# Kernel optimization log

Measured on AMD Instinct MI355X. Metric: run time of the kernel, lower is better.

The kernel has to match this reference:

```python
import jax, jax.numpy as jnp
import numpy as np

K = 3000          # number of clusters (init default)
K_SPARSE = 128    # top-k sparsification width (sparse_dim / cluster_config.k_sparse)
LR = 0.2          # EMA learning rate used in train()
EPS = 1e-12       # F.normalize eps


def setup_inputs() -> dict:
    key = jax.random.key(0)
    kx, km = jax.random.split(key)
    x = jax.random.normal(kx, (65536, 768), dtype=jnp.float32)
    mu = jax.random.normal(km, (K, 768), dtype=jnp.float32)
    mu = mu / jnp.maximum(jnp.linalg.norm(mu, axis=-1, keepdims=True), EPS)
    return {"x": x, "mu": mu}


def reference(x, mu):
    k, d = mu.shape
    # train() appends the current centers to each batch so no cluster is empty
    data = jnp.concatenate([x, mu], axis=0)            # (n+k, d)
    n_tot = data.shape[0]

    # get_r: inner-product argmax assignment
    sim = data @ mu.T                                  # (n+k, k)
    r = jnp.argmax(sim, axis=1)
    r = r.at[-k:].set(jnp.arange(k))                   # force one member per cluster

    # get_mu, vectorized: segment mean that drops the LAST member when count > 1
    ones = jnp.ones((n_tot,), dtype=data.dtype)
    counts = jax.ops.segment_sum(ones, r, num_segments=k)          # (k,)
    sums = jax.ops.segment_sum(data, r, num_segments=k)            # (k, d)
    last_idx = jax.ops.segment_max(jnp.arange(n_tot), r, num_segments=k)
    x_last = data[last_idx]                                        # (k, d)
    cnt = counts[:, None]
    u = jnp.where(cnt > 1,
                  (sums - x_last) / jnp.maximum(cnt - 1.0, 1.0),
                  sums / jnp.maximum(cnt, 1.0))

    # EMA update + normalize
    u = u * LR + mu * (1.0 - LR)
    u = u / jnp.maximum(jnp.linalg.norm(u, axis=-1, keepdims=True), EPS)

    # top_k_sparse(u, K_SPARSE).to_dense(): keep top-K_SPARSE entries by magnitude per row
    th = jax.lax.top_k(jnp.abs(u), K_SPARSE)[0][:, -1:]            # (k, 1)
    u = jnp.where(jnp.abs(u) >= th, u, jnp.zeros((), u.dtype))

    dis = jnp.max(jnp.linalg.norm(u - mu, axis=-1))
    return u, dis
```

## Files before the change

### kernel.cpp

```cpp
#include <hip/hip_runtime.h>
#include <hip/hip_bf16.h>

#define M 65536
#define N 3000
#define NPAD 3072
#define K 768
#define NT_K 24
#define NTIL 24
#define KSP 128
#define MAXL 8192
#define GAPTHR 8e-3f
#define MAXAMB 16384
#define MAXWL 196608
#define NEGINF -3.4e38f

typedef __attribute__((ext_vector_type(8))) _Float16 f16x8;
typedef __attribute__((ext_vector_type(4))) float f32x4;
typedef unsigned long long u64;
typedef unsigned int u32;

#define AS1 __attribute__((address_space(1)))
#define AS3 __attribute__((address_space(3)))

#define OFF_A2   0ull
#define OFF_B2   100663296ull
#define OFF_GTOP 105381888ull
#define OFF_RB   130547712ull
#define OFF_R    131072000ull
#define OFF_AMB  131334144ull
#define OFF_WL   131465216ull
#define OFF_CNT  132251648ull
#define WS_NEED  132251904ull

__device__ inline unsigned short f2h(float x) {
  _Float16 h = (_Float16)x;
  return *reinterpret_cast<unsigned short*>(&h);
}
__device__ inline u32 fkey(float v) {
  u32 ub = __float_as_uint(v);
  return (ub & 0x80000000u) ? ~ub : (ub | 0x80000000u);
}
__device__ inline float keyf(u32 key) {
  u32 ub = (key & 0x80000000u) ? (key ^ 0x80000000u) : ~key;
  return __uint_as_float(ub);
}
__device__ inline void gload16(const void* g, void* l) {
  __builtin_amdgcn_global_load_lds((AS1 u32*)g, (AS3 u32*)l, 16, 0, 0);
}

__global__ __launch_bounds__(256) void k_convx(const float* __restrict__ X,
                                               unsigned short* __restrict__ A2) {
  const int tot = M * (K / 8);
  for (int i = blockIdx.x * 256 + threadIdx.x; i < tot; i += gridDim.x * 256) {
    size_t base = (size_t)i * 8;
    float4 v0 = *reinterpret_cast<const float4*>(X + base);
    float4 v1 = *reinterpret_cast<const float4*>(X + base + 4);
    ushort4 h0, h1;
    h0.x = f2h(v0.x); h0.y = f2h(v0.y); h0.z = f2h(v0.z); h0.w = f2h(v0.w);
    h1.x = f2h(v1.x); h1.y = f2h(v1.y); h1.z = f2h(v1.z); h1.w = f2h(v1.w);
    *reinterpret_cast<ushort4*>(A2 + base) = h0;
    *reinterpret_cast<ushort4*>(A2 + base + 4) = h1;
  }
}

__global__ __launch_bounds__(256) void k_convmu(const float* __restrict__ MU,
                                                unsigned short* __restrict__ B2,
                                                u32* __restrict__ cnts,
                                                float* __restrict__ dis_slot) {
  int j = blockIdx.x, t = threadIdx.x;
  if (j == 0 && t == 0) { cnts[0] = 0u; cnts[1] = 0u; }
  if (j == 0 && t == 1) *dis_slot = 0.0f;
  for (int c = t; c < K; c += 256) {
    float x = (j < N) ? MU[(size_t)j * K + c] : 0.0f;
    B2[(size_t)j * K + c] = f2h(x);
  }
}

__global__ __launch_bounds__(256, 4) void k_gemm(const unsigned short* __restrict__ A2,
                                                 const unsigned short* __restrict__ B2,
                                                 u64* __restrict__ gtop) {
  __shared__ unsigned short smem[16384];

  const int bid = blockIdx.x;
  const int xcd = bid & 7, idx = bid >> 3;
  const int g = idx / 96, rem = idx % 96;
  const int nt = rem >> 2, mi = rem & 3;
  const int mt = xcd * 64 + g * 4 + mi;
  const int m0 = mt * 128, n0 = nt * 128;

  const int t = threadIdx.x;
  const int w = t >> 6, ln = t & 63;
  const int wr = w >> 1, wc = w & 1;
  const int li = ln & 15, lg = ln >> 4;

  const int r0 = t >> 2;
  const int c0 = ((t & 3) ^ ((t >> 3) & 3)) * 8;
  const unsigned short* pa0 = A2 + (size_t)(m0 + r0) * K + c0;
  const unsigned short* pb0 = B2 + (size_t)(n0 + r0) * K + c0;

  f32x4 acc[4][4] = {};

  const int rA = wr * 64 + li;
  const int rB = wc * 64 + li;
  const int cc = (lg ^ ((li >> 1) & 3)) * 8;

#define STAGE(kt_, p_)                                                        \
  {                                                                           \
    int k0_ = (kt_) * 32;                                                     \
    gload16(pa0 + k0_, smem + (p_) * 4096 + t * 8);                           \
    gload16(pa0 + (size_t)64 * K + k0_, smem + (p_) * 4096 + 2048 + t * 8);   \
    gload16(pb0 + k0_, smem + 8192 + (p_) * 4096 + t * 8);                    \
    gload16(pb0 + (size_t)64 * K + k0_,                                       \
            smem + 8192 + (p_) * 4096 + 2048 + t * 8);                        \
  }

  STAGE(0, 0);
  STAGE(1, 1);

  for (int kt = 0; kt < NT_K; ++kt) {
    const int p = kt & 1;
    if (kt >= NT_K - 1)
      asm volatile("s_waitcnt vmcnt(0)" ::: "memory");
    else
      asm volatile("s_waitcnt vmcnt(4)" ::: "memory");
    __builtin_amdgcn_s_barrier();
    asm volatile("" ::: "memory");

    const unsigned short* baseA = smem + p * 4096;
    const unsigned short* baseB = smem + 8192 + p * 4096;
    f16x8 aa[4], bb[4];
#pragma unroll
    for (int n_ = 0; n_ < 4; ++n_)
      bb[n_] = *reinterpret_cast<const f16x8*>(baseB + (rB + n_ * 16) * 32 + cc);
#pragma unroll
    for (int m_ = 0; m_ < 4; ++m_)
      aa[m_] = *reinterpret_cast<const f16x8*>(baseA + (rA + m_ * 16) * 32 + cc);

    __builtin_amdgcn_s_setprio(1);
#pragma unroll
    for (int m_ = 0; m_ < 4; ++m_)
#pragma unroll
      for (int n_ = 0; n_ < 4; ++n_)
        acc[m_][n_] = __builtin_amdgcn_mfma_f32_16x16x32_f16(
            aa[m_], bb[n_], acc[m_][n_], 0, 0, 0);
    __builtin_amdgcn_s_setprio(0);

    asm volatile("s_waitcnt lgkmcnt(0)" ::: "memory");
    __builtin_amdgcn_s_barrier();
    asm volatile("" ::: "memory");
    if (kt < NT_K - 2) STAGE(kt + 2, p);
  }

  u64* stop = reinterpret_cast<u64*>(smem);
#pragma unroll
  for (int m = 0; m < 4; ++m)
#pragma unroll
    for (int reg = 0; reg < 4; ++reg) {
      float l1 = NEGINF, l2 = NEGINF;
      int nb = 0;
#pragma unroll
      for (int n = 0; n < 4; ++n) {
        int col = n0 + wc * 64 + n * 16 + li;
        float v = (col < N) ? acc[m][n][reg] : NEGINF;
        if (v > l1) { l2 = l1; l1 = v; nb = n; }
        else if (v > l2) l2 = v;
      }
      const float loc1 = l1;
#pragma unroll
      for (int s = 1; s < 16; s <<= 1) {
        float o1 = __shfl_xor(l1, s, 64);
        float o2 = __shfl_xor(l2, s, 64);
        float hi = fmaxf(l1, o1);
        float lo = fminf(l1, o1);
        l2 = fmaxf(lo, fmaxf(l2, o2));
        l1 = hi;
      }
      unsigned long long bal = __ballot(loc1 == l1);
      unsigned mask16 = (unsigned)(bal >> (lg * 16)) & 0xffffu;
      int first = __builtin_ctz(mask16 | 0x10000u);
      int nbo = __shfl(nb, lg * 16 + first, 64);
      int col1 = n0 + wc * 64 + nbo * 16 + first;
      if (li == 0) {
        int rloc = wr * 64 + m * 16 + lg * 4 + reg;
        stop[(wc * 128 + rloc) * 2 + 0] =
            ((u64)fkey(l1) << 32) | (u32)(~(u32)col1);
        stop[(wc * 128 + rloc) * 2 + 1] = ((u64)fkey(l2) << 32);
      }
    }
  __syncthreads();
  if (t < 128) {
    u64 g1 = 0, g2 = 0;
#pragma unroll
    for (int q = 0; q < 2; ++q) {
      u64 a1 = stop[(q * 128 + t) * 2 + 0], a2 = stop[(q * 128 + t) * 2 + 1];
      u64 n1 = g1 > a1 ? g1 : a1;
      u64 lo = g1 > a1 ? a1 : g1;
      u64 mx = g2 > a2 ? g2 : a2;
      g2 = lo > mx ? lo : mx;
      g1 = n1;
    }
    u64* dst = gtop + ((size_t)(m0 + t) * NTIL + nt) * 2;
    dst[0] = g1;
    dst[1] = g2;
  }
}

__global__ __launch_bounds__(256) void k_reduce(const u64* __restrict__ gtop,
                                                int* __restrict__ r,
                                                int* __restrict__ amb,
                                                u64* __restrict__ rbest,
                                                u32* __restrict__ wl,
                                                u32* __restrict__ cnts) {
  int row = blockIdx.x * 256 + threadIdx.x;
  if (row >= M) return;
  const u64* src = gtop + (size_t)row * NTIL * 2;
  u64 tops[NTIL];
  u64 g1 = 0, g2 = 0;
#pragma unroll
  for (int tt = 0; tt < NTIL; ++tt) {
    u64 a1 = src[tt * 2], a2 = src[tt * 2 + 1];
    tops[tt] = a1;
    u64 n1 = g1 > a1 ? g1 : a1;
    u64 lo = g1 > a1 ? a1 : g1;
    u64 mx = g2 > a2 ? g2 : a2;
    g2 = lo > mx ? lo : mx;
    g1 = n1;
  }
  r[row] = (int)(~(u32)(g1 & 0xffffffffull));
  float v1 = keyf((u32)(g1 >> 32)), v2 = keyf((u32)(g2 >> 32));
  if (v1 - v2 < GAPTHR) {
    u32 idx = atomicAdd(&cnts[0], 1u);
    if (idx < MAXAMB) {
      amb[idx] = row;
      rbest[row] = 0ull;
      float thr = v1 - GAPTHR;
#pragma unroll
      for (int tt = 0; tt < NTIL; ++tt) {
        if (keyf((u32)(tops[tt] >> 32)) >= thr) {
          u32 wi = atomicAdd(&cnts[1], 1u);
          if (wi < MAXWL) wl[wi] = ((u32)row << 5) | (u32)tt;
        }
      }
    }
  }
}

__global__ __launch_bounds__(256) void k_refine(const float* __restrict__ X,
                                                const float* __restrict__ MU,
                                                const u32* __restrict__ wl,
                                                const u32* __restrict__ cnts,
                                                u64* __restrict__ rbest) {
  __shared__ float xrow[768];
  __shared__ u64 wb[4];
  const int t = threadIdx.x, w = t >> 6, ln = t & 63;
  const int nw = (int)min(cnts[1], (u32)MAXWL);
  for (int u = blockIdx.x; u < nw; u += gridDim.x) {
    const u32 e = wl[u];
    const int row = (int)(e >> 5), tile = (int)(e & 31);

    xrow[t] = X[(size_t)row * K + t];
    xrow[t + 256] = X[(size_t)row * K + t + 256];
    xrow[t + 512] = X[(size_t)row * K + t + 512];
    __syncthreads();

    u64 best = 0;
    for (int q = 0; q < 8; ++q) {
      const int cbase = tile * 128 + w * 32 + q * 4;
      const float* m0p = MU + (size_t)min(cbase + 0, N - 1) * K;
      const float* m1p = MU + (size_t)min(cbase + 1, N - 1) * K;
      const float* m2p = MU + (size_t)min(cbase + 2, N - 1) * K;
      const float* m3p = MU + (size_t)min(cbase + 3, N - 1) * K;
      float p0 = 0.f, p1 = 0.f, p2 = 0.f, p3 = 0.f;
#pragma unroll
      for (int it = 0; it < 3; ++it) {
        int d4 = (ln + it * 64) * 4;
        float4 xv = *reinterpret_cast<const float4*>(&xrow[d4]);
        float4 a0 = *reinterpret_cast<const float4*>(m0p + d4);
        float4 a1 = *reinterpret_cast<const float4*>(m1p + d4);
        float4 a2 = *reinterpret_cast<const float4*>(m2p + d4);
        float4 a3 = *reinterpret_cast<const float4*>(m3p + d4);
        p0 += xv.x * a0.x + xv.y * a0.y + xv.z * a0.z + xv.w * a0.w;
        p1 += xv.x * a1.x + xv.y * a1.y + xv.z * a1.z + xv.w * a1.w;
        p2 += xv.x * a2.x + xv.y * a2.y + xv.z * a2.z + xv.w * a2.w;
        p3 += xv.x * a3.x + xv.y * a3.y + xv.z * a3.z + xv.w * a3.w;
      }
#pragma unroll
      for (int s = 32; s; s >>= 1) {
        p0 += __shfl_xor(p0, s, 64);
        p1 += __shfl_xor(p1, s, 64);
        p2 += __shfl_xor(p2, s, 64);
        p3 += __shfl_xor(p3, s, 64);
      }
      if (ln == 0) {
        float ps[4] = {p0, p1, p2, p3};
#pragma unroll
        for (int i = 0; i < 4; ++i) {
          int c = cbase + i;
          if (c < N) {
            u64 pk = ((u64)fkey(ps[i]) << 32) | (u32)(~(u32)c);
            if (pk > best) best = pk;
          }
        }
      }
    }
    if (ln == 0) wb[w] = best;
    __syncthreads();
    if (t == 0) {
      u64 b = wb[0];
#pragma unroll
      for (int i = 1; i < 4; ++i)
        if (wb[i] > b) b = wb[i];
      atomicMax(&rbest[row], b);
    }
    __syncthreads();
  }
}

__global__ __launch_bounds__(256) void k_decode2(const int* __restrict__ amb,
                                                 const u64* __restrict__ rbest,
                                                 const u32* __restrict__ cnts,
                                                 int* __restrict__ r) {
  int i = blockIdx.x * 256 + threadIdx.x;
  int n_amb = (int)min(cnts[0], (u32)MAXAMB);
  if (i < n_amb) {
    int row = amb[i];
    r[row] = (int)(~(u32)(rbest[row] & 0xffffffffull));
  }
}

__global__ __launch_bounds__(256) void k_finalize(const float* __restrict__ X,
                                                  const float* __restrict__ MU,
                                                  const int* __restrict__ r,
                                                  float* __restrict__ out,
                                                  float* __restrict__ dis_slot) {
#pragma clang fp contract(off)
  const int j = blockIdx.x;
  const int t = threadIdx.x;
  const int lane = t & 63;
  const int wid = t >> 6;
  __shared__ int list[MAXL];
  __shared__ int wc4[4][4];
  __shared__ float red[4];
  __shared__ unsigned hist[256];
  __shared__ int selI;

  int cnt = 0;
  for (int base = 0; base < M; base += 1024) {
    bool f[4];
    u64 bm[4];
#pragma unroll
    for (int q = 0; q < 4; ++q) {
      f[q] = (r[base + q * 256 + t] == j);
      bm[q] = __ballot(f[q]);
    }
    if (lane == 0) {
#pragma unroll
      for (int q = 0; q < 4; ++q) wc4[wid][q] = __popcll(bm[q]);
    }
    __syncthreads();
    int goff = cnt;
#pragma unroll
    for (int q = 0; q < 4; ++q) {
      if (f[q]) {
        int off = goff;
        for (int ww = 0; ww < wid; ++ww) off += wc4[ww][q];
        int pos = off + __popcll(bm[q] & ((1ull << lane) - 1ull));
        if (pos < MAXL) list[pos] = base + q * 256 + t;
      }
      goff += wc4[0][q] + wc4[1][q] + wc4[2][q] + wc4[3][q];
    }
    cnt = goff;
    __syncthreads();
  }
  int cl = cnt < MAXL ? cnt : MAXL;

  float a0 = 0.f, a1 = 0.f, a2 = 0.f, a3 = 0.f;
  float b0 = 0.f, b1 = 0.f, b2 = 0.f, b3 = 0.f;
  float c0 = 0.f, c1 = 0.f, c2 = 0.f, c3 = 0.f;
  int m = 0;
  for (; m + 3 < cl; m += 4) {
    const float* x0 = X + (size_t)list[m + 0] * K;
    const float* x1 = X + (size_t)list[m + 1] * K;
    const float* x2 = X + (size_t)list[m + 2] * K;
    const float* x3 = X + (size_t)list[m + 3] * K;
    a0 += x0[t]; b0 += x0[t + 256]; c0 += x0[t + 512];
    a1 += x1[t]; b1 += x1[t + 256]; c1 += x1[t + 512];
    a2 += x2[t]; b2 += x2[t + 256]; c2 += x2[t + 512];
    a3 += x3[t]; b3 += x3[t + 256]; c3 += x3[t + 512];
  }
  for (; m < cl; ++m) {
    const float* xr = X + (size_t)list[m] * K;
    a0 += xr[t]; b0 += xr[t + 256]; c0 += xr[t + 512];
  }
  float s0 = ((a0 + a1) + a2) + a3;
  float s1 = ((b0 + b1) + b2) + b3;
  float s2 = ((c0 + c1) + c2) + c3;

  const float mu0 = MU[(size_t)j * K + t];
  const float mu1 = MU[(size_t)j * K + t + 256];
  const float mu2 = MU[(size_t)j * K + t + 512];

  float u0, u1, u2;
  if (cnt >= 1) {
    float c = (float)cnt;
    u0 = s0 / c; u1 = s1 / c; u2 = s2 / c;
  } else {
    u0 = mu0; u1 = mu1; u2 = mu2;
  }
  float v0 = u0 * 0.2f + mu0 * 0.8f;
  float v1 = u1 * 0.2f + mu1 * 0.8f;
  float v2 = u2 * 0.2f + mu2 * 0.8f;

  float ss = v0 * v0 + v1 * v1 + v2 * v2;
#pragma unroll
  for (int s = 32; s > 0; s >>= 1) ss += __shfl_down(ss, s, 64);
  if (lane == 0) red[wid] = ss;
  __syncthreads();
  float tot = red[0] + red[1] + red[2] + red[3];
  float den = sqrtf(tot);
  den = fmaxf(den, 1e-12f);
  float un0 = v0 / den, un1 = v1 / den, un2 = v2 / den;
  unsigned k0b = __float_as_uint(fabsf(un0));
  unsigned k1b = __float_as_uint(fabsf(un1));
  unsigned k2b = __float_as_uint(fabsf(un2));
  __syncthreads();

  unsigned cur = 0;
  int need = KSP;
  for (int sh = 24; sh >= 0; sh -= 8) {
    hist[t] = 0u;
    if (t == 0) selI = -1;
    __syncthreads();
    bool m0_ = (sh == 24) || ((k0b >> (sh + 8)) == (cur >> (sh + 8)));
    bool m1_ = (sh == 24) || ((k1b >> (sh + 8)) == (cur >> (sh + 8)));
    bool m2_ = (sh == 24) || ((k2b >> (sh + 8)) == (cur >> (sh + 8)));
    if (m0_) atomicAdd(&hist[(k0b >> sh) & 255u], 1u);
    if (m1_) atomicAdd(&hist[(k1b >> sh) & 255u], 1u);
    if (m2_) atomicAdd(&hist[(k2b >> sh) & 255u], 1u);
    __syncthreads();
#pragma unroll
    for (int off = 1; off < 256; off <<= 1) {
      unsigned nb = (t + off < 256) ? hist[t + off] : 0u;
      __syncthreads();
      hist[t] += nb;
      __syncthreads();
    }
    if (hist[t] >= (unsigned)need) atomicMax(&selI, t);
    __syncthreads();
    int b = selI < 0 ? 0 : selI;
    unsigned above = (b < 255) ? hist[b + 1] : 0u;
    cur |= ((unsigned)b << sh);
    need = need - (int)above;
    __syncthreads();
  }
  unsigned th = cur;

  float o0 = (k0b >= th) ? un0 : 0.0f;
  float o1 = (k1b >= th) ? un1 : 0.0f;
  float o2 = (k2b >= th) ? un2 : 0.0f;
  out[(size_t)j * K + t] = o0;
  out[(size_t)j * K + t + 256] = o1;
  out[(size_t)j * K + t + 512] = o2;

  float q0 = o0 - mu0, q1 = o1 - mu1, q2 = o2 - mu2;
  float dq = q0 * q0 + q1 * q1 + q2 * q2;
#pragma unroll
  for (int s = 32; s > 0; s >>= 1) dq += __shfl_down(dq, s, 64);
  __syncthreads();
  if (lane == 0) red[wid] = dq;
  __syncthreads();
  if (t == 0) {
    float dtot = red[0] + red[1] + red[2] + red[3];
    float dn = sqrtf(dtot);
    atomicMax((unsigned*)dis_slot, __float_as_uint(dn));
  }
}

__global__ __launch_bounds__(256) void k0_init(u64* __restrict__ best,
                                               float* __restrict__ dis_slot) {
  int i = blockIdx.x * 256 + threadIdx.x;
  if (i < M) best[i] = 0ull;
  if (i == 0) *dis_slot = 0.0f;
}

__global__ __launch_bounds__(256) void k1_f32(const float* __restrict__ X,
                                              const float* __restrict__ MU,
                                              u64* __restrict__ best) {
  __shared__ float Asf[16][64];
  __shared__ float Bsf[16][64];
  const int m0 = blockIdx.x * 64;
  const int n0 = blockIdx.y * 64;
  const int t = threadIdx.x;
  const int tx = t & 15, ty = t >> 4;
  const int lrow = t >> 2, lcg = t & 3;

  float acc[4][4];
#pragma unroll
  for (int i = 0; i < 4; ++i)
#pragma unroll
    for (int jj = 0; jj < 4; ++jj) acc[i][jj] = 0.0f;

  const float* aptr = X + (size_t)(m0 + lrow) * K + lcg * 4;
  const bool bvalid = (n0 + lrow) < N;
  const float* bptr = MU + (size_t)(bvalid ? (n0 + lrow) : 0) * K + lcg * 4;

  for (int k0 = 0; k0 < K; k0 += 16) {
    float4 av = *reinterpret_cast<const float4*>(aptr + k0);
    float4 bv = make_float4(0.f, 0.f, 0.f, 0.f);
    if (bvalid) bv = *reinterpret_cast<const float4*>(bptr + k0);
    Asf[lcg * 4 + 0][lrow] = av.x; Asf[lcg * 4 + 1][lrow] = av.y;
    Asf[lcg * 4 + 2][lrow] = av.z; Asf[lcg * 4 + 3][lrow] = av.w;
    Bsf[lcg * 4 + 0][lrow] = bv.x; Bsf[lcg * 4 + 1][lrow] = bv.y;
    Bsf[lcg * 4 + 2][lrow] = bv.z; Bsf[lcg * 4 + 3][lrow] = bv.w;
    __syncthreads();
#pragma unroll
    for (int kk = 0; kk < 16; ++kk) {
      float4 af = *reinterpret_cast<const float4*>(&Asf[kk][ty * 4]);
      float4 bf = *reinterpret_cast<const float4*>(&Bsf[kk][tx * 4]);
      float a[4] = {af.x, af.y, af.z, af.w};
      float b[4] = {bf.x, bf.y, bf.z, bf.w};
#pragma unroll
      for (int i = 0; i < 4; ++i)
#pragma unroll
        for (int jj = 0; jj < 4; ++jj)
          acc[i][jj] = fmaf(a[i], b[jj], acc[i][jj]);
    }
    __syncthreads();
  }
#pragma unroll
  for (int i = 0; i < 4; ++i) {
    u64 bk = 0ull;
#pragma unroll
    for (int jj = 0; jj < 4; ++jj) {
      int col = n0 + tx * 4 + jj;
      if (col < N) {
        u64 pk = ((u64)fkey(acc[i][jj]) << 32) | (u32)(~(u32)col);
        if (pk > bk) bk = pk;
      }
    }
#pragma unroll
    for (int s = 1; s < 16; s <<= 1) {
      u64 o = __shfl_xor((unsigned long long)bk, s, 64);
      if (o > bk) bk = o;
    }
    if (tx == 0) atomicMax(&best[m0 + ty * 4 + i], bk);
  }
}

__global__ __launch_bounds__(256) void k2_decode(const u64* __restrict__ best,
                                                 int* __restrict__ r) {
  int i = blockIdx.x * 256 + threadIdx.x;
  if (i < M) r[i] = (int)(~(u32)(best[i] & 0xffffffffull));
}

extern "C" void kernel_launch(void* const* d_in, const int* in_sizes, int n_in,
                              void* d_out, int out_size, void* d_ws, size_t ws_size,
                              hipStream_t stream) {
  const float* X = (const float*)d_in[0];
  const float* MU = (const float*)d_in[1];
  float* out = (float*)d_out;
  float* dis_slot = out + (size_t)N * K;

  if (ws_size >= WS_NEED) {
    unsigned short* A2 = (unsigned short*)((char*)d_ws + OFF_A2);
    unsigned short* B2 = (unsigned short*)((char*)d_ws + OFF_B2);
    u64* gtop = (u64*)((char*)d_ws + OFF_GTOP);
    u64* rbest = (u64*)((char*)d_ws + OFF_RB);
    int* r = (int*)((char*)d_ws + OFF_R);
    int* amb = (int*)((char*)d_ws + OFF_AMB);
    u32* wl = (u32*)((char*)d_ws + OFF_WL);
    u32* cnts = (u32*)((char*)d_ws + OFF_CNT);

    k_convx<<<8192, 256, 0, stream>>>(X, A2);
    k_convmu<<<NPAD, 256, 0, stream>>>(MU, B2, cnts, dis_slot);
    k_gemm<<<512 * NTIL, 256, 0, stream>>>(A2, B2, gtop);
    k_reduce<<<M / 256, 256, 0, stream>>>(gtop, r, amb, rbest, wl, cnts);
    k_refine<<<2048, 256, 0, stream>>>(X, MU, wl, cnts, rbest);
    k_decode2<<<MAXAMB / 256, 256, 0, stream>>>(amb, rbest, cnts, r);
    k_finalize<<<N, 256, 0, stream>>>(X, MU, r, out, dis_slot);
  } else {
    u64* best = (u64*)d_ws;
    int* r = (int*)((char*)d_ws + (size_t)M * sizeof(u64));
    k0_init<<<M / 256, 256, 0, stream>>>(best, dis_slot);
    dim3 g1(M / 64, (N + 63) / 64);
    k1_f32<<<g1, 256, 0, stream>>>(X, MU, best);
    k2_decode<<<M / 256, 256, 0, stream>>>(best, r);
    k_finalize<<<N, 256, 0, stream>>>(X, MU, r, out, dis_slot);
  }
}
```

Baseline: 796.7 us.

## Skip empty row chunks in finalize via per-cluster chunk bitmaps; tighten ambiguity gap

Adds a per-cluster 64-bit bitmap recording which 1024-row chunks hold members. It is set with atomicOr in the reduce and decode kernels, and finalize scans only the chunks that have members instead of all 65536 assignments for each of the 3000 clusters. This removes most of finalize's full scan of r, which each block previously repeated. It also lowers the gap threshold for ambiguous rows, so fewer rows go through fp32 refinement. That risks argmax mismatches where the fp16 GEMM error exceeds the tighter gap. Stale bits are harmless because a chunk whose row was reassigned is scanned and simply matches nothing.

```diff
diff --git a/kernel.cpp b/kernel.cpp
--- a/kernel.cpp
+++ b/kernel.cpp
@@ -9,7 +9,7 @@
 #define NTIL 24
 #define KSP 128
 #define MAXL 8192
-#define GAPTHR 8e-3f
+#define GAPTHR 4.5e-3f
 #define MAXAMB 16384
 #define MAXWL 196608
 #define NEGINF -3.4e38f
@@ -30,7 +30,8 @@
 #define OFF_AMB  131334144ull
 #define OFF_WL   131465216ull
 #define OFF_CNT  132251648ull
-#define WS_NEED  132251904ull
+#define OFF_CM   132251904ull
+#define WS_NEED  132276480ull
 
 __device__ inline unsigned short f2h(float x) {
   _Float16 h = (_Float16)x;
@@ -66,10 +67,12 @@
 __global__ __launch_bounds__(256) void k_convmu(const float* __restrict__ MU,
                                                 unsigned short* __restrict__ B2,
                                                 u32* __restrict__ cnts,
+                                                u64* __restrict__ chunkmap,
                                                 float* __restrict__ dis_slot) {
   int j = blockIdx.x, t = threadIdx.x;
   if (j == 0 && t == 0) { cnts[0] = 0u; cnts[1] = 0u; }
   if (j == 0 && t == 1) *dis_slot = 0.0f;
+  if (t == 2 && j < N) chunkmap[j] = 0ull;
   for (int c = t; c < K; c += 256) {
     float x = (j < N) ? MU[(size_t)j * K + c] : 0.0f;
     B2[(size_t)j * K + c] = f2h(x);
@@ -210,7 +213,8 @@
                                                 int* __restrict__ amb,
                                                 u64* __restrict__ rbest,
                                                 u32* __restrict__ wl,
-                                                u32* __restrict__ cnts) {
+                                                u32* __restrict__ cnts,
+                                                u64* __restrict__ chunkmap) {
   int row = blockIdx.x * 256 + threadIdx.x;
   if (row >= M) return;
   const u64* src = gtop + (size_t)row * NTIL * 2;
@@ -226,7 +230,9 @@
     g2 = lo > mx ? lo : mx;
     g1 = n1;
   }
-  r[row] = (int)(~(u32)(g1 & 0xffffffffull));
+  int jbest = (int)(~(u32)(g1 & 0xffffffffull));
+  r[row] = jbest;
+  atomicOr(&chunkmap[jbest], 1ull << (row >> 10));
   float v1 = keyf((u32)(g1 >> 32)), v2 = keyf((u32)(g2 >> 32));
   if (v1 - v2 < GAPTHR) {
     u32 idx = atomicAdd(&cnts[0], 1u);
@@ -319,18 +325,22 @@
 __global__ __launch_bounds__(256) void k_decode2(const int* __restrict__ amb,
                                                  const u64* __restrict__ rbest,
                                                  const u32* __restrict__ cnts,
-                                                 int* __restrict__ r) {
+                                                 int* __restrict__ r,
+                                                 u64* __restrict__ chunkmap) {
   int i = blockIdx.x * 256 + threadIdx.x;
   int n_amb = (int)min(cnts[0], (u32)MAXAMB);
   if (i < n_amb) {
     int row = amb[i];
-    r[row] = (int)(~(u32)(rbest[row] & 0xffffffffull));
+    int jn = (int)(~(u32)(rbest[row] & 0xffffffffull));
+    r[row] = jn;
+    atomicOr(&chunkmap[jn], 1ull << (row >> 10));
   }
 }
 
 __global__ __launch_bounds__(256) void k_finalize(const float* __restrict__ X,
                                                   const float* __restrict__ MU,
                                                   const int* __restrict__ r,
+                                                  const u64* __restrict__ chunkmap,
                                                   float* __restrict__ out,
                                                   float* __restrict__ dis_slot) {
 #pragma clang fp contract(off)
@@ -344,8 +354,11 @@
   __shared__ unsigned hist[256];
   __shared__ int selI;
 
+  const u64 cmap = chunkmap[j];
   int cnt = 0;
-  for (int base = 0; base < M; base += 1024) {
+  for (int ch = 0; ch < 64; ++ch) {
+    if (!((cmap >> ch) & 1ull)) continue;
+    const int base = ch << 10;
     bool f[4];
     u64 bm[4];
 #pragma unroll
@@ -553,6 +566,11 @@
   if (i < M) r[i] = (int)(~(u32)(best[i] & 0xffffffffull));
 }
 
+__global__ __launch_bounds__(256) void k_mapall(u64* __restrict__ chunkmap) {
+  int i = blockIdx.x * 256 + threadIdx.x;
+  if (i < N) chunkmap[i] = ~0ull;
+}
+
 extern "C" void kernel_launch(void* const* d_in, const int* in_sizes, int n_in,
                               void* d_out, int out_size, void* d_ws, size_t ws_size,
                               hipStream_t stream) {
@@ -570,21 +588,24 @@
     int* amb = (int*)((char*)d_ws + OFF_AMB);
     u32* wl = (u32*)((char*)d_ws + OFF_WL);
     u32* cnts = (u32*)((char*)d_ws + OFF_CNT);
+    u64* chunkmap = (u64*)((char*)d_ws + OFF_CM);
 
     k_convx<<<8192, 256, 0, stream>>>(X, A2);
-    k_convmu<<<NPAD, 256, 0, stream>>>(MU, B2, cnts, dis_slot);
+    k_convmu<<<NPAD, 256, 0, stream>>>(MU, B2, cnts, chunkmap, dis_slot);
     k_gemm<<<512 * NTIL, 256, 0, stream>>>(A2, B2, gtop);
-    k_reduce<<<M / 256, 256, 0, stream>>>(gtop, r, amb, rbest, wl, cnts);
+    k_reduce<<<M / 256, 256, 0, stream>>>(gtop, r, amb, rbest, wl, cnts, chunkmap);
     k_refine<<<2048, 256, 0, stream>>>(X, MU, wl, cnts, rbest);
-    k_decode2<<<MAXAMB / 256, 256, 0, stream>>>(amb, rbest, cnts, r);
-    k_finalize<<<N, 256, 0, stream>>>(X, MU, r, out, dis_slot);
+    k_decode2<<<MAXAMB / 256, 256, 0, stream>>>(amb, rbest, cnts, r, chunkmap);
+    k_finalize<<<N, 256, 0, stream>>>(X, MU, r, chunkmap, out, dis_slot);
   } else {
     u64* best = (u64*)d_ws;
     int* r = (int*)((char*)d_ws + (size_t)M * sizeof(u64));
+    u64* chunkmap = (u64*)((char*)d_ws + (size_t)M * 12);
     k0_init<<<M / 256, 256, 0, stream>>>(best, dis_slot);
+    k_mapall<<<(N + 255) / 256, 256, 0, stream>>>(chunkmap);
     dim3 g1(M / 64, (N + 63) / 64);
     k1_f32<<<g1, 256, 0, stream>>>(X, MU, best);
     k2_decode<<<M / 256, 256, 0, stream>>>(best, r);
-    k_finalize<<<N, 256, 0, stream>>>(X, MU, r, out, dis_slot);
-  }
-}
+    k_finalize<<<N, 256, 0, stream>>>(X, MU, r, chunkmap, out, dis_slot);
+  }
+}
```

After: 650.6 us, median of 2. 1.22x faster.
